# Kernel tuning notes

Hardware: AMD Instinct MI355X
Metric: run time of the kernel (lower is better)

The kernel has to match this reference:

```python
import jax, jax.numpy as jnp
import numpy as np
import math

HEAD_N = 8
IN_FEATS = 512
BATCH, LENG = 4, 2048
LN_EPS = 1e-5


def setup_inputs() -> dict:
    key = jax.random.key(0)
    ks = jax.random.split(key, 16)
    d = IN_FEATS
    inp = {
        "q": jax.random.normal(ks[0], (BATCH, LENG, d), jnp.float32),
        "k": jax.random.normal(ks[1], (BATCH, LENG, d), jnp.float32),
        "v": jax.random.normal(ks[2], (BATCH, LENG, d), jnp.float32),
        # 4 Linear(in_feats, in_feats): weights [out,in] torch-style, bias [out]
        "Wq": jax.random.normal(ks[3], (d, d), jnp.float32) * 0.02,
        "bq": jnp.zeros((d,), jnp.float32),
        "Wk": jax.random.normal(ks[4], (d, d), jnp.float32) * 0.02,
        "bk": jnp.zeros((d,), jnp.float32),
        "Wv": jax.random.normal(ks[5], (d, d), jnp.float32) * 0.02,
        "bv": jnp.zeros((d,), jnp.float32),
        "Wo": jax.random.normal(ks[6], (d, d), jnp.float32) * 0.02,
        "bo": jnp.zeros((d,), jnp.float32),
        "gamma": jnp.ones((d,), jnp.float32),
        "beta": jnp.zeros((d,), jnp.float32),
    }
    return inp


def _split_heads(x, W, b):
    # Linear then reshape exactly as the torch code: (B,L,D)->(B,L,H,dh)->(B,H,L,dh)->(B*H,L,dh)
    B, L, D = x.shape
    dh = D // HEAD_N
    y = x @ W.T + b
    y = y.reshape(B, L, HEAD_N, dh).transpose(0, 2, 1, 3).reshape(B * HEAD_N, L, dh)
    return y


def reference(q, k, v, Wq, bq, Wk, bk, Wv, bv, Wo, bo, gamma, beta):
    residual = q
    B, L, D = q.shape
    dh = D // HEAD_N
    qh = _split_heads(q, Wq, bq)  # [B*H, L, dh]
    kh = _split_heads(k, Wk, bk)
    vh = _split_heads(v, Wv, bv)

    scores = jnp.einsum("nqd,nkd->nqk", qh, kh) / math.sqrt(dh)  # [B*H, L, L]
    raw_att = jax.nn.softmax(scores, axis=-1)
    att = jnp.einsum("nqk,nkd->nqd", raw_att, vh)  # [B*H, L, dh]

    # Faithful to the original (buggy) merge: reshape (B*H,L,dh) AS IF layout were (H,B,L,dh)
    att = att.reshape(HEAD_N, B, L, dh).transpose(1, 2, 0, 3).reshape(B, L, D)

    att = att @ Wo.T + bo
    # dropout is identity in eval/reference mode
    x = att + residual
    mu = jnp.mean(x, axis=-1, keepdims=True)
    var = jnp.mean(jnp.square(x - mu), axis=-1, keepdims=True)
    out = (x - mu) / jnp.sqrt(var + LN_EPS) * gamma + beta
    return (out, raw_att)
```

## Files before the change

### kernel.cpp

```cpp
#include <hip/hip_runtime.h>
#include <hip/hip_bf16.h>

#define D_MODEL 512
#define SEQ 2048
#define NB 4
#define NH 8
#define DH 64
#define NHEADS 32
#define MROWS 8192

typedef __bf16 bf16_t;
typedef __bf16 bf16x4_t __attribute__((ext_vector_type(4)));
typedef __bf16 bf16x8_t __attribute__((ext_vector_type(8)));
typedef float f32x4_t __attribute__((ext_vector_type(4)));

__device__ inline f32x4_t mfma16(bf16x8_t a, bf16x8_t b, f32x4_t c) {
    return __builtin_amdgcn_mfma_f32_16x16x32_bf16(a, b, c, 0, 0, 0);
}

__global__ __launch_bounds__(256) void qkv_proj_all_kernel(
    const float* __restrict__ qp, const float* __restrict__ kp, const float* __restrict__ vp,
    const float* __restrict__ Wq, const float* __restrict__ bq,
    const float* __restrict__ Wk, const float* __restrict__ bk,
    const float* __restrict__ Wv, const float* __restrict__ bv,
    bf16_t* __restrict__ qfrag, bf16_t* __restrict__ kfrag, bf16_t* __restrict__ vfrag)
{
    __shared__ bf16_t As[128][72];
    __shared__ bf16_t Bs[128][72];

    const int mode = blockIdx.z;
    const float* X    = (mode == 0) ? qp : (mode == 1) ? kp : vp;
    const float* W    = (mode == 0) ? Wq : (mode == 1) ? Wk : Wv;
    const float* bias = (mode == 0) ? bq : (mode == 1) ? bk : bv;
    bf16_t* dst       = (mode == 0) ? qfrag : (mode == 1) ? kfrag : vfrag;

    const int t = threadIdx.x;
    const int lane = t & 63, w = t >> 6;
    const int lr = lane & 15, lg = lane >> 4;
    const int wm = w >> 1, wn = w & 1;
    const int m0 = blockIdx.x * 128, n0 = blockIdx.y * 128;

    f32x4_t acc[4][4];
#pragma unroll
    for (int i = 0; i < 4; i++)
#pragma unroll
        for (int j = 0; j < 4; j++) acc[i][j] = f32x4_t{0.f, 0.f, 0.f, 0.f};

    const int srow = t >> 4;
    const int scol = (t & 15) * 4;

    bf16_t (*Pa)[72] = (mode == 2) ? As : Bs;
    bf16_t (*Pb)[72] = (mode == 2) ? Bs : As;

    for (int kt = 0; kt < 8; kt++) {
        __syncthreads();
#pragma unroll
        for (int p = 0; p < 8; p++) {
            int row = p * 16 + srow;
            float4 va = *(const float4*)(X + (size_t)(m0 + row) * 512 + kt * 64 + scol);
            bf16x4_t ha = { (bf16_t)va.x, (bf16_t)va.y, (bf16_t)va.z, (bf16_t)va.w };
            *(bf16x4_t*)(&As[row][scol]) = ha;
            float4 vb = *(const float4*)(W + (size_t)(n0 + row) * 512 + kt * 64 + scol);
            bf16x4_t hb = { (bf16_t)vb.x, (bf16_t)vb.y, (bf16_t)vb.z, (bf16_t)vb.w };
            *(bf16x4_t*)(&Bs[row][scol]) = hb;
        }
        __syncthreads();
#pragma unroll
        for (int kk = 0; kk < 64; kk += 32) {
            bf16x8_t fa[4], fb[4];
#pragma unroll
            for (int i = 0; i < 4; i++)
                fa[i] = *(const bf16x8_t*)(&Pa[wm * 64 + i * 16 + lr][kk + lg * 8]);
#pragma unroll
            for (int j = 0; j < 4; j++)
                fb[j] = *(const bf16x8_t*)(&Pb[wn * 64 + j * 16 + lr][kk + lg * 8]);
#pragma unroll
            for (int i = 0; i < 4; i++)
#pragma unroll
                for (int j = 0; j < 4; j++)
                    acc[i][j] = mfma16(fa[i], fb[j], acc[i][j]);
        }
    }

    if (mode == 2) {
#pragma unroll
        for (int j = 0; j < 4; j++) {
            int col = n0 + wn * 64 + j * 16 + lr;
            float bval = bias[col];
            int h = col >> 6, d = col & 63;
#pragma unroll
            for (int i = 0; i < 4; i++) {
                int rbase = m0 + wm * 64 + i * 16 + lg * 4;
                int b = rbase >> 11, l0 = rbase & 2047;
                int win = l0 >> 5, kkg = l0 & 31;
                int pos0 = (kkg < 16) ? ((kkg >> 2) * 8) : (((kkg - 16) >> 2) * 8 + 4);
                bf16x4_t hv;
#pragma unroll
                for (int r = 0; r < 4; r++) hv[r] = (bf16_t)(acc[i][j][r] + bval);
                *(bf16x4_t*)(dst + ((((size_t)(b * NH + h) * 64 + win) * 64 + d) * 32 + pos0)) = hv;
            }
        }
    } else {
#pragma unroll
        for (int i = 0; i < 4; i++) {
            int featbase = n0 + wm * 64 + i * 16 + lg * 4;
            float4 b4 = *(const float4*)(bias + featbase);
            float bb[4] = { b4.x, b4.y, b4.z, b4.w };
            int h = featbase >> 6, d0 = featbase & 63;
            int c = (d0 & 31) >> 3, e0 = d0 & 7, fd = (d0 >= 32) ? 1 : 0;
#pragma unroll
            for (int j = 0; j < 4; j++) {
                int seq = m0 + wn * 64 + j * 16 + lr;
                int b = seq >> 11, l = seq & 2047;
                bf16x4_t hv;
#pragma unroll
                for (int r = 0; r < 4; r++) hv[r] = (bf16_t)(acc[i][j][r] + bb[r]);
                size_t idx;
                if (mode == 0) {
                    int qw = l >> 4, lp = (l & 15) + 16 * c;
                    idx = ((((size_t)(b * NH + h) * 128 + qw) * 2 + fd) * 64 + lp) * 8 + e0;
                } else {
                    int win = l >> 5, fk = (((l & 31) >= 16) ? 2 : 0) + fd;
                    int lp = (l & 15) + 16 * c;
                    idx = ((((size_t)(b * NH + h) * 64 + win) * 4 + fk) * 64 + lp) * 8 + e0;
                }
                *(bf16x4_t*)(dst + idx) = hv;
            }
        }
    }
}

__global__ __launch_bounds__(256, 2) void attn_kernel(
    const bf16_t* __restrict__ qfrag, const bf16_t* __restrict__ kfrag,
    const bf16_t* __restrict__ vfrag, float* __restrict__ probs,
    bf16_t* __restrict__ attw)
{
    __shared__ float stage[4][16][132];

    const int bh = blockIdx.y;
    const int t = threadIdx.x;
    const int lane = t & 63, w = t >> 6;
    const int lr = lane & 15, lg = lane >> 4;
    const int q0c0 = blockIdx.x * 128 + w * 32;
    const int q0c1 = q0c0 + 16;
    const int qw0 = q0c0 >> 4;

    const bf16_t* qfb = qfrag + (size_t)bh * 131072;
    const bf16x8_t qA0 = *(const bf16x8_t*)(qfb + ((size_t)(qw0 * 2 + 0) * 64 + lane) * 8);
    const bf16x8_t qA1 = *(const bf16x8_t*)(qfb + ((size_t)(qw0 * 2 + 1) * 64 + lane) * 8);
    const bf16x8_t qB0 = *(const bf16x8_t*)(qfb + ((size_t)(qw0 * 2 + 2) * 64 + lane) * 8);
    const bf16x8_t qB1 = *(const bf16x8_t*)(qfb + ((size_t)(qw0 * 2 + 3) * 64 + lane) * 8);

    const bf16_t* kfb = kfrag + (size_t)bh * 131072;
    const bf16_t* vfb = vfrag + (size_t)bh * 131072;

    float sum0 = 0.f;
    {
        const bf16_t* kp0 = kfb + lane * 8;
        bf16x8_t k00 = *(const bf16x8_t*)(kp0);
        bf16x8_t k01 = *(const bf16x8_t*)(kp0 + 512);
        bf16x8_t k10 = *(const bf16x8_t*)(kp0 + 1024);
        bf16x8_t k11 = *(const bf16x8_t*)(kp0 + 1536);
#pragma unroll 2
        for (int win = 0; win < 64; win++) {
            bf16x8_t n00 = k00, n01 = k01, n10 = k10, n11 = k11;
            if (win < 63) {
                const bf16_t* kp = kfb + (size_t)(win + 1) * 2048 + lane * 8;
                n00 = *(const bf16x8_t*)(kp);
                n01 = *(const bf16x8_t*)(kp + 512);
                n10 = *(const bf16x8_t*)(kp + 1024);
                n11 = *(const bf16x8_t*)(kp + 1536);
            }
            f32x4_t s0 = {0.f, 0.f, 0.f, 0.f}, s1 = {0.f, 0.f, 0.f, 0.f};
            s0 = mfma16(k00, qA0, s0);
            s0 = mfma16(k01, qA1, s0);
            s1 = mfma16(k10, qA0, s1);
            s1 = mfma16(k11, qA1, s1);
#pragma unroll
            for (int r = 0; r < 4; r++)
                sum0 += __expf(s0[r] * 0.125f) + __expf(s1[r] * 0.125f);
            k00 = n00; k01 = n01; k10 = n10; k11 = n11;
        }
    }
    sum0 += __shfl_xor(sum0, 16, 64);
    sum0 += __shfl_xor(sum0, 32, 64);
    const float ri0 = 1.0f / sum0;

    f32x4_t oacc[4];
#pragma unroll
    for (int db = 0; db < 4; db++) oacc[db] = f32x4_t{0.f, 0.f, 0.f, 0.f};
    float sum1 = 0.f;
    {
        float* pb = probs + (size_t)bh * SEQ * SEQ + (size_t)q0c0 * SEQ;
        const bf16_t* kp0 = kfb + lane * 8;
        bf16x8_t k00 = *(const bf16x8_t*)(kp0);
        bf16x8_t k01 = *(const bf16x8_t*)(kp0 + 512);
        bf16x8_t k10 = *(const bf16x8_t*)(kp0 + 1024);
        bf16x8_t k11 = *(const bf16x8_t*)(kp0 + 1536);

        for (int sw = 0; sw < 16; sw++) {
#pragma unroll
            for (int c = 0; c < 4; c++) {
                const int win = sw * 4 + c;
                bf16x8_t av[4];
#pragma unroll
                for (int db = 0; db < 4; db++)
                    av[db] = *(const bf16x8_t*)(vfb + (((size_t)win * 64 + db * 16 + lr) * 32 + lg * 8));
                bf16x8_t n00 = k00, n01 = k01, n10 = k10, n11 = k11;
                if (win < 63) {
                    const bf16_t* kp = kfb + (size_t)(win + 1) * 2048 + lane * 8;
                    n00 = *(const bf16x8_t*)(kp);
                    n01 = *(const bf16x8_t*)(kp + 512);
                    n10 = *(const bf16x8_t*)(kp + 1024);
                    n11 = *(const bf16x8_t*)(kp + 1536);
                }
                f32x4_t s0 = {0.f, 0.f, 0.f, 0.f}, s1 = {0.f, 0.f, 0.f, 0.f};
                s0 = mfma16(k00, qA0, s0);
                s0 = mfma16(k01, qA1, s0);
                s1 = mfma16(k10, qA0, s1);
                s1 = mfma16(k11, qA1, s1);
                float pl[8];
#pragma unroll
                for (int r = 0; r < 4; r++) {
                    pl[r]     = __expf(s0[r] * 0.125f) * ri0;
                    pl[4 + r] = __expf(s1[r] * 0.125f) * ri0;
                }
                const int c0_ = c * 32;
                f32x4_t lo = { pl[0], pl[1], pl[2], pl[3] };
                f32x4_t hi = { pl[4], pl[5], pl[6], pl[7] };
                *(f32x4_t*)(&stage[w][lr][c0_ + lg * 4])      = lo;
                *(f32x4_t*)(&stage[w][lr][c0_ + 16 + lg * 4]) = hi;
                bf16x8_t p;
#pragma unroll
                for (int e = 0; e < 8; e++) p[e] = (bf16_t)pl[e];
#pragma unroll
                for (int db = 0; db < 4; db++)
                    oacc[db] = mfma16(av[db], p, oacc[db]);
                f32x4_t u0 = {0.f, 0.f, 0.f, 0.f}, u1 = {0.f, 0.f, 0.f, 0.f};
                u0 = mfma16(k00, qB0, u0);
                u0 = mfma16(k01, qB1, u0);
                u1 = mfma16(k10, qB0, u1);
                u1 = mfma16(k11, qB1, u1);
#pragma unroll
                for (int r = 0; r < 4; r++)
                    sum1 += __expf(u0[r] * 0.125f) + __expf(u1[r] * 0.125f);
                k00 = n00; k01 = n01; k10 = n10; k11 = n11;
            }
#pragma unroll
            for (int it = 0; it < 8; it++) {
                int row = it * 2 + (lane >> 5);
                int col = (lane & 31) * 4;
                f32x4_t vv = *(const f32x4_t*)(&stage[w][row][col]);
                __builtin_nontemporal_store(vv, (f32x4_t*)(pb + (size_t)row * SEQ + sw * 128 + col));
            }
        }
    }
    sum1 += __shfl_xor(sum1, 16, 64);
    sum1 += __shfl_xor(sum1, 32, 64);
    const float ri1 = 1.0f / sum1;

    {
        float* ow = &stage[w][0][0];
#pragma unroll
        for (int db = 0; db < 4; db++)
#pragma unroll
            for (int r = 0; r < 4; r++)
                ow[(db * 16 + lg * 4 + r) * 17 + lr] = oacc[db][r];
        bf16x8_t h0, h1;
#pragma unroll
        for (int jj = 0; jj < 8; jj++) h0[jj] = (bf16_t)ow[(lg * 16 + jj) * 17 + lr];
#pragma unroll
        for (int jj = 0; jj < 8; jj++) h1[jj] = (bf16_t)ow[(lg * 16 + 8 + jj) * 17 + lr];
        bf16_t* ao = attw + ((size_t)bh * SEQ + q0c0 + lr) * DH + lg * 16;
        *(bf16x8_t*)(ao)     = h0;
        *(bf16x8_t*)(ao + 8) = h1;
    }

#pragma unroll
    for (int db = 0; db < 4; db++) oacc[db] = f32x4_t{0.f, 0.f, 0.f, 0.f};
    {
        float* pb = probs + (size_t)bh * SEQ * SEQ + (size_t)q0c1 * SEQ;
        const bf16_t* kp0 = kfb + lane * 8;
        bf16x8_t k00 = *(const bf16x8_t*)(kp0);
        bf16x8_t k01 = *(const bf16x8_t*)(kp0 + 512);
        bf16x8_t k10 = *(const bf16x8_t*)(kp0 + 1024);
        bf16x8_t k11 = *(const bf16x8_t*)(kp0 + 1536);

        for (int sw = 0; sw < 16; sw++) {
#pragma unroll
            for (int c = 0; c < 4; c++) {
                const int win = sw * 4 + c;
                bf16x8_t av[4];
#pragma unroll
                for (int db = 0; db < 4; db++)
                    av[db] = *(const bf16x8_t*)(vfb + (((size_t)win * 64 + db * 16 + lr) * 32 + lg * 8));
                bf16x8_t n00 = k00, n01 = k01, n10 = k10, n11 = k11;
                if (win < 63) {
                    const bf16_t* kp = kfb + (size_t)(win + 1) * 2048 + lane * 8;
                    n00 = *(const bf16x8_t*)(kp);
                    n01 = *(const bf16x8_t*)(kp + 512);
                    n10 = *(const bf16x8_t*)(kp + 1024);
                    n11 = *(const bf16x8_t*)(kp + 1536);
                }
                f32x4_t s0 = {0.f, 0.f, 0.f, 0.f}, s1 = {0.f, 0.f, 0.f, 0.f};
                s0 = mfma16(k00, qB0, s0);
                s0 = mfma16(k01, qB1, s0);
                s1 = mfma16(k10, qB0, s1);
                s1 = mfma16(k11, qB1, s1);
                float pl[8];
#pragma unroll
                for (int r = 0; r < 4; r++) {
                    pl[r]     = __expf(s0[r] * 0.125f) * ri1;
                    pl[4 + r] = __expf(s1[r] * 0.125f) * ri1;
                }
                const int c0_ = c * 32;
                f32x4_t lo = { pl[0], pl[1], pl[2], pl[3] };
                f32x4_t hi = { pl[4], pl[5], pl[6], pl[7] };
                *(f32x4_t*)(&stage[w][lr][c0_ + lg * 4])      = lo;
                *(f32x4_t*)(&stage[w][lr][c0_ + 16 + lg * 4]) = hi;
                bf16x8_t p;
#pragma unroll
                for (int e = 0; e < 8; e++) p[e] = (bf16_t)pl[e];
#pragma unroll
                for (int db = 0; db < 4; db++)
                    oacc[db] = mfma16(av[db], p, oacc[db]);
                k00 = n00; k01 = n01; k10 = n10; k11 = n11;
            }
#pragma unroll
            for (int it = 0; it < 8; it++) {
                int row = it * 2 + (lane >> 5);
                int col = (lane & 31) * 4;
                f32x4_t vv = *(const f32x4_t*)(&stage[w][row][col]);
                __builtin_nontemporal_store(vv, (f32x4_t*)(pb + (size_t)row * SEQ + sw * 128 + col));
            }
        }
    }

    {
        float* ow = &stage[w][0][0];
#pragma unroll
        for (int db = 0; db < 4; db++)
#pragma unroll
            for (int r = 0; r < 4; r++)
                ow[(db * 16 + lg * 4 + r) * 17 + lr] = oacc[db][r];
        bf16x8_t h0, h1;
#pragma unroll
        for (int jj = 0; jj < 8; jj++) h0[jj] = (bf16_t)ow[(lg * 16 + jj) * 17 + lr];
#pragma unroll
        for (int jj = 0; jj < 8; jj++) h1[jj] = (bf16_t)ow[(lg * 16 + 8 + jj) * 17 + lr];
        bf16_t* ao = attw + ((size_t)bh * SEQ + q0c1 + lr) * DH + lg * 16;
        *(bf16x8_t*)(ao)     = h0;
        *(bf16x8_t*)(ao + 8) = h1;
    }
}

__global__ __launch_bounds__(256, 2) void out_ln_kernel(
    const bf16_t* __restrict__ attw, const float* __restrict__ Wo,
    const float* __restrict__ bo, const float* __restrict__ resid,
    const float* __restrict__ gamma, const float* __restrict__ beta,
    float* __restrict__ out)
{
    __shared__ __align__(16) char smem[78336];
    bf16_t (*As)[72] = (bf16_t(*)[72])smem;
    bf16_t (*Bs)[72] = (bf16_t(*)[72])(smem + 4608);
    float  (*ow)[516] = (float(*)[516])smem;

    const int t = threadIdx.x;
    const int lane = t & 63, w = t >> 6;
    const int lr = lane & 15, lg = lane >> 4;
    const int wr = w >> 1, wc = w & 1;
    const int m0 = blockIdx.x * 32;

    f32x4_t acc[16];
#pragma unroll
    for (int j = 0; j < 16; j++) acc[j] = f32x4_t{0.f, 0.f, 0.f, 0.f};

    for (int kt = 0; kt < 8; kt++) {
        __syncthreads();
        {
            int row = t >> 3, d0 = (t & 7) * 8;
            int grow = m0 + row;
            int b = grow >> 11, l = grow & 2047;
            bf16x8_t va = *(const bf16x8_t*)(attw + (size_t)((kt * NB + b) * SEQ + l) * DH + d0);
            *(bf16x8_t*)(&As[row][d0]) = va;
        }
#pragma unroll
        for (int p = 0; p < 8; p++) {
            int row = p * 64 + (t >> 2);
            int c0 = (t & 3) * 16;
            const float* wp = Wo + (size_t)row * 512 + kt * 64 + c0;
#pragma unroll
            for (int it = 0; it < 4; it++) {
                float4 v4 = *(const float4*)(wp + it * 4);
                bf16x4_t hb = { (bf16_t)v4.x, (bf16_t)v4.y, (bf16_t)v4.z, (bf16_t)v4.w };
                *(bf16x4_t*)(&Bs[row][c0 + it * 4]) = hb;
            }
        }
        __syncthreads();
#pragma unroll
        for (int kk = 0; kk < 64; kk += 32) {
            bf16x8_t af = *(const bf16x8_t*)(&As[wr * 16 + lr][kk + lg * 8]);
#pragma unroll
            for (int j = 0; j < 16; j++) {
                bf16x8_t bfr = *(const bf16x8_t*)(&Bs[wc * 256 + j * 16 + lr][kk + lg * 8]);
                acc[j] = mfma16(af, bfr, acc[j]);
            }
        }
    }

    __syncthreads();
#pragma unroll
    for (int j = 0; j < 16; j++)
#pragma unroll
        for (int r = 0; r < 4; r++)
            ow[wr * 16 + lg * 4 + r][wc * 256 + j * 16 + lr] = acc[j][r];
    __syncthreads();

    const int hrow = lane >> 5;
    const int c0 = (lane & 31) * 4;
#pragma unroll
    for (int rp = 0; rp < 4; rp++) {
        int row = w * 8 + rp * 2 + hrow;
        int grow = m0 + row;
        const float* rr = resid + (size_t)grow * 512;
        f32x4_t x[4];
        float s = 0.f, sq = 0.f;
#pragma unroll
        for (int it = 0; it < 4; it++) {
            f32x4_t oy = *(const f32x4_t*)(&ow[row][c0 + it * 128]);
            f32x4_t bb = *(const f32x4_t*)(bo + c0 + it * 128);
            f32x4_t qv = *(const f32x4_t*)(rr + c0 + it * 128);
            f32x4_t xv = { oy[0] + bb[0] + qv[0], oy[1] + bb[1] + qv[1],
                           oy[2] + bb[2] + qv[2], oy[3] + bb[3] + qv[3] };
            x[it] = xv;
#pragma unroll
            for (int e = 0; e < 4; e++) { s += xv[e]; sq += xv[e] * xv[e]; }
        }
#pragma unroll
        for (int msk = 16; msk >= 1; msk >>= 1) {
            s  += __shfl_xor(s,  msk, 64);
            sq += __shfl_xor(sq, msk, 64);
        }
        float mean = s * (1.f / 512.f);
        float var  = sq * (1.f / 512.f) - mean * mean;
        float rstd = rsqrtf(var + 1e-5f);
        float* op = out + (size_t)grow * 512;
#pragma unroll
        for (int it = 0; it < 4; it++) {
            f32x4_t gv = *(const f32x4_t*)(gamma + c0 + it * 128);
            f32x4_t bv = *(const f32x4_t*)(beta + c0 + it * 128);
            f32x4_t ov;
#pragma unroll
            for (int e = 0; e < 4; e++)
                ov[e] = (x[it][e] - mean) * rstd * gv[e] + bv[e];
            *(f32x4_t*)(op + c0 + it * 128) = ov;
        }
    }
}

extern "C" void kernel_launch(void* const* d_in, const int* in_sizes, int n_in,
                              void* d_out, int out_size, void* d_ws, size_t ws_size,
                              hipStream_t stream)
{
    (void)in_sizes; (void)n_in; (void)out_size; (void)ws_size;

    const float* q     = (const float*)d_in[0];
    const float* k     = (const float*)d_in[1];
    const float* v     = (const float*)d_in[2];
    const float* Wq    = (const float*)d_in[3];
    const float* bq    = (const float*)d_in[4];
    const float* Wk    = (const float*)d_in[5];
    const float* bk    = (const float*)d_in[6];
    const float* Wv    = (const float*)d_in[7];
    const float* bv    = (const float*)d_in[8];
    const float* Wo    = (const float*)d_in[9];
    const float* bo    = (const float*)d_in[10];
    const float* gamma = (const float*)d_in[11];
    const float* beta  = (const float*)d_in[12];

    float* out   = (float*)d_out;
    float* probs = out + (size_t)NB * SEQ * D_MODEL;

    char* ws = (char*)d_ws;
    bf16_t* qfrag = (bf16_t*)(ws);
    bf16_t* kfrag = (bf16_t*)(ws + 8388608);
    bf16_t* vfrag = (bf16_t*)(ws + 16777216);
    bf16_t* attw  = (bf16_t*)(ws + 25165824);

    qkv_proj_all_kernel<<<dim3(64, 4, 3), 256, 0, stream>>>(
        q, k, v, Wq, bq, Wk, bk, Wv, bv, qfrag, kfrag, vfrag);
    attn_kernel<<<dim3(16, 32), 256, 0, stream>>>(qfrag, kfrag, vfrag, probs, attw);
    out_ln_kernel<<<256, 256, 0, stream>>>(attw, Wo, bo, q, gamma, beta, out);
}
```

Before: 212.0 us.

## Pre-pack Wo into MFMA fragment layout and drop LDS staging in out-proj

Adds a fourth z-slice to the projection kernel that converts Wo to bf16 once and writes it in MFMA B-fragment order. The output projection then loads A and B fragments straight from global memory, with no LDS tiles and no per-tile barriers. This removes the redundant fp32-to-bf16 conversion of Wo that each of the 256 blocks did before. In exchange every wave re-reads the packed weights from global/L2, with no shared-memory reuse across waves.

```diff
diff --git a/kernel.cpp b/kernel.cpp
--- a/kernel.cpp
+++ b/kernel.cpp
@@ -23,18 +23,39 @@
     const float* __restrict__ Wq, const float* __restrict__ bq,
     const float* __restrict__ Wk, const float* __restrict__ bk,
     const float* __restrict__ Wv, const float* __restrict__ bv,
-    bf16_t* __restrict__ qfrag, bf16_t* __restrict__ kfrag, bf16_t* __restrict__ vfrag)
+    const float* __restrict__ Wo,
+    bf16_t* __restrict__ qfrag, bf16_t* __restrict__ kfrag,
+    bf16_t* __restrict__ vfrag, bf16_t* __restrict__ wofrag)
 {
     __shared__ bf16_t As[128][72];
     __shared__ bf16_t Bs[128][72];
 
     const int mode = blockIdx.z;
+    const int t = threadIdx.x;
+
+    if (mode == 3) {
+        int gid = ((blockIdx.y * 64 + blockIdx.x) * 256 + t);
+        if (gid < 32768) {
+            int ktkk = gid >> 11;
+            int cb   = (gid >> 6) & 31;
+            int lane = gid & 63;
+            int col  = cb * 16 + (lane & 15);
+            int k0   = (ktkk >> 1) * 64 + (ktkk & 1) * 32 + (lane >> 4) * 8;
+            const float* wp = Wo + (size_t)col * 512 + k0;
+            float4 v0 = *(const float4*)(wp);
+            float4 v1 = *(const float4*)(wp + 4);
+            bf16x8_t hv = { (bf16_t)v0.x, (bf16_t)v0.y, (bf16_t)v0.z, (bf16_t)v0.w,
+                            (bf16_t)v1.x, (bf16_t)v1.y, (bf16_t)v1.z, (bf16_t)v1.w };
+            *(bf16x8_t*)(wofrag + (size_t)gid * 8) = hv;
+        }
+        return;
+    }
+
     const float* X    = (mode == 0) ? qp : (mode == 1) ? kp : vp;
     const float* W    = (mode == 0) ? Wq : (mode == 1) ? Wk : Wv;
     const float* bias = (mode == 0) ? bq : (mode == 1) ? bk : bv;
     bf16_t* dst       = (mode == 0) ? qfrag : (mode == 1) ? kfrag : vfrag;
 
-    const int t = threadIdx.x;
     const int lane = t & 63, w = t >> 6;
     const int lr = lane & 15, lg = lane >> 4;
     const int wm = w >> 1, wn = w & 1;
@@ -355,15 +376,12 @@
 }
 
 __global__ __launch_bounds__(256, 2) void out_ln_kernel(
-    const bf16_t* __restrict__ attw, const float* __restrict__ Wo,
+    const bf16_t* __restrict__ attw, const bf16_t* __restrict__ wofrag,
     const float* __restrict__ bo, const float* __restrict__ resid,
     const float* __restrict__ gamma, const float* __restrict__ beta,
     float* __restrict__ out)
 {
-    __shared__ __align__(16) char smem[78336];
-    bf16_t (*As)[72] = (bf16_t(*)[72])smem;
-    bf16_t (*Bs)[72] = (bf16_t(*)[72])(smem + 4608);
-    float  (*ow)[516] = (float(*)[516])smem;
+    __shared__ float ow[32][516];
 
     const int t = threadIdx.x;
     const int lane = t & 63, w = t >> 6;
@@ -371,44 +389,28 @@
     const int wr = w >> 1, wc = w & 1;
     const int m0 = blockIdx.x * 32;
 
+    const int grow = m0 + wr * 16 + lr;
+    const int b = grow >> 11, l = grow & 2047;
+
     f32x4_t acc[16];
 #pragma unroll
     for (int j = 0; j < 16; j++) acc[j] = f32x4_t{0.f, 0.f, 0.f, 0.f};
 
+#pragma unroll 1
     for (int kt = 0; kt < 8; kt++) {
-        __syncthreads();
-        {
-            int row = t >> 3, d0 = (t & 7) * 8;
-            int grow = m0 + row;
-            int b = grow >> 11, l = grow & 2047;
-            bf16x8_t va = *(const bf16x8_t*)(attw + (size_t)((kt * NB + b) * SEQ + l) * DH + d0);
-            *(bf16x8_t*)(&As[row][d0]) = va;
-        }
-#pragma unroll
-        for (int p = 0; p < 8; p++) {
-            int row = p * 64 + (t >> 2);
-            int c0 = (t & 3) * 16;
-            const float* wp = Wo + (size_t)row * 512 + kt * 64 + c0;
-#pragma unroll
-            for (int it = 0; it < 4; it++) {
-                float4 v4 = *(const float4*)(wp + it * 4);
-                bf16x4_t hb = { (bf16_t)v4.x, (bf16_t)v4.y, (bf16_t)v4.z, (bf16_t)v4.w };
-                *(bf16x4_t*)(&Bs[row][c0 + it * 4]) = hb;
-            }
-        }
-        __syncthreads();
-#pragma unroll
-        for (int kk = 0; kk < 64; kk += 32) {
-            bf16x8_t af = *(const bf16x8_t*)(&As[wr * 16 + lr][kk + lg * 8]);
+#pragma unroll
+        for (int kk = 0; kk < 2; kk++) {
+            bf16x8_t af = *(const bf16x8_t*)(
+                attw + (size_t)((kt * NB + b) * SEQ + l) * DH + kk * 32 + lg * 8);
+            const bf16_t* wb = wofrag + (((size_t)(kt * 2 + kk) * 32 + wc * 16) * 64) * 8;
 #pragma unroll
             for (int j = 0; j < 16; j++) {
-                bf16x8_t bfr = *(const bf16x8_t*)(&Bs[wc * 256 + j * 16 + lr][kk + lg * 8]);
+                bf16x8_t bfr = *(const bf16x8_t*)(wb + ((size_t)j * 64 + lane) * 8);
                 acc[j] = mfma16(af, bfr, acc[j]);
             }
         }
     }
 
-    __syncthreads();
 #pragma unroll
     for (int j = 0; j < 16; j++)
 #pragma unroll
@@ -421,8 +423,8 @@
 #pragma unroll
     for (int rp = 0; rp < 4; rp++) {
         int row = w * 8 + rp * 2 + hrow;
-        int grow = m0 + row;
-        const float* rr = resid + (size_t)grow * 512;
+        int gr = m0 + row;
+        const float* rr = resid + (size_t)gr * 512;
         f32x4_t x[4];
         float s = 0.f, sq = 0.f;
 #pragma unroll
@@ -444,7 +446,7 @@
         float mean = s * (1.f / 512.f);
         float var  = sq * (1.f / 512.f) - mean * mean;
         float rstd = rsqrtf(var + 1e-5f);
-        float* op = out + (size_t)grow * 512;
+        float* op = out + (size_t)gr * 512;
 #pragma unroll
         for (int it = 0; it < 4; it++) {
             f32x4_t gv = *(const f32x4_t*)(gamma + c0 + it * 128);
@@ -482,13 +484,14 @@
     float* probs = out + (size_t)NB * SEQ * D_MODEL;
 
     char* ws = (char*)d_ws;
-    bf16_t* qfrag = (bf16_t*)(ws);
-    bf16_t* kfrag = (bf16_t*)(ws + 8388608);
-    bf16_t* vfrag = (bf16_t*)(ws + 16777216);
-    bf16_t* attw  = (bf16_t*)(ws + 25165824);
-
-    qkv_proj_all_kernel<<<dim3(64, 4, 3), 256, 0, stream>>>(
-        q, k, v, Wq, bq, Wk, bk, Wv, bv, qfrag, kfrag, vfrag);
+    bf16_t* qfrag  = (bf16_t*)(ws);
+    bf16_t* kfrag  = (bf16_t*)(ws + 8388608);
+    bf16_t* vfrag  = (bf16_t*)(ws + 16777216);
+    bf16_t* attw   = (bf16_t*)(ws + 25165824);
+    bf16_t* wofrag = (bf16_t*)(ws + 33554432);
+
+    qkv_proj_all_kernel<<<dim3(64, 4, 4), 256, 0, stream>>>(
+        q, k, v, Wq, bq, Wk, bk, Wv, bv, Wo, qfrag, kfrag, vfrag, wofrag);
     attn_kernel<<<dim3(16, 32), 256, 0, stream>>>(qfrag, kfrag, vfrag, probs, attw);
-    out_ln_kernel<<<256, 256, 0, stream>>>(attw, Wo, bo, q, gamma, beta, out);
+    out_ln_kernel<<<256, 256, 0, stream>>>(attw, wofrag, bo, q, gamma, beta, out);
 }
```

Result: no change. 214.8 us (+1.4%).
